# Performance work log

Measured on AMD Instinct MI355X. Metric: run time of the kernel, lower is better.

Reference implementation:

```python
import jax, jax.numpy as jnp
import numpy as np

BS, LX, LY, H, MD = 16, 1024, 1024, 512, 512


def setup_inputs() -> dict:
    key = jax.random.key(0)
    ks = jax.random.split(key, 8)
    x = jax.random.normal(ks[0], (BS, LX, H), dtype=jnp.float32)
    y = jax.random.normal(ks[1], (BS, LY, H), dtype=jnp.float32)
    y_mask = jax.random.bernoulli(ks[2], 0.2, (BS, LY))  # True = masked
    s1 = 1.0 / np.sqrt(H)
    W1 = jax.random.uniform(ks[3], (MD, H), jnp.float32, -s1, s1)
    b1 = jax.random.uniform(ks[4], (MD,), jnp.float32, -s1, s1)
    W2 = jax.random.uniform(ks[5], (MD, H), jnp.float32, -s1, s1)
    b2 = jax.random.uniform(ks[6], (MD,), jnp.float32, -s1, s1)
    s2 = 1.0 / np.sqrt(MD)
    k7, k8 = jax.random.split(ks[7])
    w_o = jax.random.uniform(k7, (MD,), jnp.float32, -s2, s2)
    b_o = jax.random.uniform(k8, (), jnp.float32, -s2, s2)
    return {"x": x, "y": y, "y_mask": y_mask, "W1": W1, "b1": b1,
            "W2": W2, "b2": b2, "w_o": w_o, "b_o": b_o}


def reference(x, y, y_mask, W1, b1, W2, b2, w_o, b_o):
    # Projections: [B,L,MD]
    x_proj = jax.nn.relu(jnp.einsum('blh,mh->blm', x, W1) + b1)
    y_proj = jax.nn.relu(jnp.einsum('blh,mh->blm', y, W2) + b2)
    # o_liner is linear, so o_liner(x_i + y_j) = w_o.x_i + w_o.y_j + b_o
    sx = x_proj @ w_o  # [B,Lx]
    sy = y_proj @ w_o  # [B,Ly]
    scores = sx[:, :, None] + sy[:, None, :] + b_o  # [B,Lx,Ly]
    scores = jnp.where(y_mask[:, None, :], jnp.float32(-1e7), scores)
    alpha = jax.nn.softmax(scores, axis=-1)  # softmax over len_y
    return alpha
```

## Files before the change

kernel.cpp:

```cpp
#include <hip/hip_runtime.h>
#include <hip/hip_bf16.h>

#define BS 16
#define LX 1024
#define LY 1024
#define H 512
#define MD 512
#define RY (BS * LY)

typedef __attribute__((ext_vector_type(8))) __bf16 bf16x8;
typedef __attribute__((ext_vector_type(4))) float floatx4;

__device__ __forceinline__ void load_lds16(const __bf16* g, __bf16* l) {
    __builtin_amdgcn_global_load_lds(
        (const __attribute__((address_space(1))) void*)g,
        (__attribute__((address_space(3))) void*)l,
        16, 0, 0);
}

__global__ __launch_bounds__(256) void prep_w2(const float* __restrict__ W2,
                                               __bf16* __restrict__ wb) {
    const int i = blockIdx.x * 256 + threadIdx.x;
    const float4 a = *(const float4*)(W2 + (size_t)i * 8);
    const float4 b = *(const float4*)(W2 + (size_t)i * 8 + 4);
    bf16x8 v = { (__bf16)a.x, (__bf16)a.y, (__bf16)a.z, (__bf16)a.w,
                 (__bf16)b.x, (__bf16)b.y, (__bf16)b.z, (__bf16)b.w };
    *(bf16x8*)(wb + (size_t)i * 8) = v;
}

#define BM 64
#define BN 128
#define BKT 64
__global__ __launch_bounds__(256) void gemm_sy(const float* __restrict__ Y,
                                               const __bf16* __restrict__ wb,
                                               const float* __restrict__ b2,
                                               const float* __restrict__ wo,
                                               float* __restrict__ part) {
    __shared__ __align__(16) __bf16 Bs[BN * BKT];

    const int tid  = threadIdx.x;
    const int lane = tid & 63;
    const int wave = tid >> 6;
    const int wm = wave >> 1;
    const int wn = wave & 1;
    const int la = lane & 15;
    const int qa = lane >> 4;

    const int id = blockIdx.x;
    const int mt = ((id >> 5) << 3) | (id & 7);
    const int nt = (id >> 3) & 3;
    const int m0 = mt * BM, n0 = nt * BN;

    const int lrow = lane >> 3;
    const int lcol = (lane & 7) * 8;

    const float* yrow0 = Y + (size_t)(m0 + wm * 32 + la) * H + qa * 8;
    const float* yrow1 = yrow0 + 16 * H;

    floatx4 acc[2][4] = {};

    for (int k0 = 0; k0 < H; k0 += BKT) {
        float4 a00 = *(const float4*)(yrow0 + k0);
        float4 a01 = *(const float4*)(yrow0 + k0 + 4);
        float4 a02 = *(const float4*)(yrow0 + k0 + 32);
        float4 a03 = *(const float4*)(yrow0 + k0 + 36);
        float4 a10 = *(const float4*)(yrow1 + k0);
        float4 a11 = *(const float4*)(yrow1 + k0 + 4);
        float4 a12 = *(const float4*)(yrow1 + k0 + 32);
        float4 a13 = *(const float4*)(yrow1 + k0 + 36);

        __syncthreads();
        #pragma unroll
        for (int r = 0; r < 4; ++r) {
            const int rb = r * 32 + wave * 8;
            load_lds16(wb + (size_t)(n0 + rb + lrow) * H + k0 + lcol, &Bs[rb * BKT]);
        }

        bf16x8 afr[2][2];
        afr[0][0] = { (__bf16)a00.x, (__bf16)a00.y, (__bf16)a00.z, (__bf16)a00.w,
                      (__bf16)a01.x, (__bf16)a01.y, (__bf16)a01.z, (__bf16)a01.w };
        afr[0][1] = { (__bf16)a02.x, (__bf16)a02.y, (__bf16)a02.z, (__bf16)a02.w,
                      (__bf16)a03.x, (__bf16)a03.y, (__bf16)a03.z, (__bf16)a03.w };
        afr[1][0] = { (__bf16)a10.x, (__bf16)a10.y, (__bf16)a10.z, (__bf16)a10.w,
                      (__bf16)a11.x, (__bf16)a11.y, (__bf16)a11.z, (__bf16)a11.w };
        afr[1][1] = { (__bf16)a12.x, (__bf16)a12.y, (__bf16)a12.z, (__bf16)a12.w,
                      (__bf16)a13.x, (__bf16)a13.y, (__bf16)a13.z, (__bf16)a13.w };

        __syncthreads();

        #pragma unroll
        for (int kh = 0; kh < 2; ++kh) {
            bf16x8 bfr[4];
            #pragma unroll
            for (int nf = 0; nf < 4; ++nf)
                bfr[nf] = *(const bf16x8*)&Bs[(wn * 64 + nf * 16 + la) * BKT + kh * 32 + qa * 8];
            #pragma unroll
            for (int mf = 0; mf < 2; ++mf)
                #pragma unroll
                for (int nf = 0; nf < 4; ++nf)
                    acc[mf][nf] = __builtin_amdgcn_mfma_f32_16x16x32_bf16(afr[mf][kh], bfr[nf], acc[mf][nf], 0, 0, 0);
        }
    }

    const int slice = nt * 2 + wn;
    #pragma unroll
    for (int mf = 0; mf < 2; ++mf) {
        #pragma unroll
        for (int reg = 0; reg < 4; ++reg) {
            float s = 0.f;
            #pragma unroll
            for (int nf = 0; nf < 4; ++nf) {
                const int n = n0 + wn * 64 + nf * 16 + la;
                float v = acc[mf][nf][reg] + b2[n];
                v = fmaxf(v, 0.f);
                s += v * wo[n];
            }
            s += __shfl_xor(s, 1);
            s += __shfl_xor(s, 2);
            s += __shfl_xor(s, 4);
            s += __shfl_xor(s, 8);
            if (la == 0) {
                const int m = m0 + wm * 32 + mf * 16 + qa * 4 + reg;
                part[(size_t)slice * RY + m] = s;
            }
        }
    }
}

__global__ __launch_bounds__(256) void softmax_p(const float* __restrict__ part,
                                                 const int* __restrict__ mask,
                                                 float* __restrict__ p) {
    const int b = blockIdx.x;
    const int tid = threadIdx.x;
    __shared__ float red[8];

    float vals[4];
    int   ms[4];
    float mx = -INFINITY;
    #pragma unroll
    for (int c = 0; c < 4; ++c) {
        const int j = c * 256 + tid;
        float v = 0.f;
        #pragma unroll
        for (int t = 0; t < 8; ++t) v += part[t * RY + b * LY + j];
        vals[c] = v;
        ms[c]   = mask[b * LY + j];
        if (!ms[c]) mx = fmaxf(mx, v);
    }
    #pragma unroll
    for (int off = 1; off < 64; off <<= 1) mx = fmaxf(mx, __shfl_xor(mx, off));
    if ((tid & 63) == 0) red[tid >> 6] = mx;
    __syncthreads();
    mx = fmaxf(fmaxf(red[0], red[1]), fmaxf(red[2], red[3]));

    float e[4];
    float sum = 0.f;
    #pragma unroll
    for (int c = 0; c < 4; ++c) {
        e[c] = ms[c] ? 0.f : __expf(vals[c] - mx);
        sum += e[c];
    }
    #pragma unroll
    for (int off = 1; off < 64; off <<= 1) sum += __shfl_xor(sum, off);
    if ((tid & 63) == 0) red[4 + (tid >> 6)] = sum;
    __syncthreads();
    sum = red[4] + red[5] + red[6] + red[7];
    const float inv = 1.0f / sum;

    #pragma unroll
    for (int c = 0; c < 4; ++c)
        p[b * LY + c * 256 + tid] = e[c] * inv;
}

__global__ __launch_bounds__(256) void bcast(const float* __restrict__ p,
                                             float4* __restrict__ out) {
    const int tid = threadIdx.x;
    const long base_row = (long)blockIdx.x * 8;
    const int b = (int)(base_row >> 10);
    const float4 v = *(const float4*)(p + b * LY + tid * 4);
    float4* o = out + base_row * (LY / 4) + tid;
    #pragma unroll
    for (int r = 0; r < 8; ++r) o[r * (LY / 4)] = v;
}

extern "C" void kernel_launch(void* const* d_in, const int* in_sizes, int n_in,
                              void* d_out, int out_size, void* d_ws, size_t ws_size,
                              hipStream_t stream) {
    const float* y  = (const float*)d_in[1];
    const int*   ym = (const int*)  d_in[2];
    const float* W2 = (const float*)d_in[5];
    const float* b2 = (const float*)d_in[6];
    const float* wo = (const float*)d_in[7];

    char* ws = (char*)d_ws;
    __bf16* wb   = (__bf16*)ws;
    float*  part = (float*)(ws + (size_t)MD * H * 2);
    float*  p    = part + 8 * RY;

    prep_w2<<<(MD * H) / (256 * 8), 256, 0, stream>>>(W2, wb);
    gemm_sy<<<(MD / BN) * (RY / BM), 256, 0, stream>>>(y, wb, b2, wo, part);
    softmax_p<<<BS, 256, 0, stream>>>(part, ym, p);
    bcast<<<(BS * LX) / 8, 256, 0, stream>>>(p, (float4*)d_out);
}
```

Measured before the change: 162.2 us.

## Double-buffer W2 tiles in LDS and XOR-swizzle layout to avoid bank conflicts

```diff
diff --git a/kernel.cpp b/kernel.cpp
--- a/kernel.cpp
+++ b/kernel.cpp
@@ -31,12 +31,13 @@
 #define BM 64
 #define BN 128
 #define BKT 64
+#define NK (H / BKT)
 __global__ __launch_bounds__(256) void gemm_sy(const float* __restrict__ Y,
                                                const __bf16* __restrict__ wb,
                                                const float* __restrict__ b2,
                                                const float* __restrict__ wo,
                                                float* __restrict__ part) {
-    __shared__ __align__(16) __bf16 Bs[BN * BKT];
+    __shared__ __align__(16) __bf16 Bs[2][BN * BKT];
 
     const int tid  = threadIdx.x;
     const int lane = tid & 63;
@@ -52,48 +53,61 @@
     const int m0 = mt * BM, n0 = nt * BN;
 
     const int lrow = lane >> 3;
-    const int lcol = (lane & 7) * 8;
+    const int lcol = (((lane & 7) ^ lrow) * 8);
 
     const float* yrow0 = Y + (size_t)(m0 + wm * 32 + la) * H + qa * 8;
     const float* yrow1 = yrow0 + 16 * H;
 
     floatx4 acc[2][4] = {};
-
-    for (int k0 = 0; k0 < H; k0 += BKT) {
-        float4 a00 = *(const float4*)(yrow0 + k0);
-        float4 a01 = *(const float4*)(yrow0 + k0 + 4);
-        float4 a02 = *(const float4*)(yrow0 + k0 + 32);
-        float4 a03 = *(const float4*)(yrow0 + k0 + 36);
-        float4 a10 = *(const float4*)(yrow1 + k0);
-        float4 a11 = *(const float4*)(yrow1 + k0 + 4);
-        float4 a12 = *(const float4*)(yrow1 + k0 + 32);
-        float4 a13 = *(const float4*)(yrow1 + k0 + 36);
-
+    float4 a[8];
+
+    a[0] = *(const float4*)(yrow0);      a[1] = *(const float4*)(yrow0 + 4);
+    a[2] = *(const float4*)(yrow0 + 32); a[3] = *(const float4*)(yrow0 + 36);
+    a[4] = *(const float4*)(yrow1);      a[5] = *(const float4*)(yrow1 + 4);
+    a[6] = *(const float4*)(yrow1 + 32); a[7] = *(const float4*)(yrow1 + 36);
+    #pragma unroll
+    for (int r = 0; r < 4; ++r) {
+        const int rb = r * 32 + wave * 8;
+        load_lds16(wb + (size_t)(n0 + rb + lrow) * H + lcol, &Bs[0][rb * BKT]);
+    }
+
+    for (int k = 0; k < NK; ++k) {
+        const int cur = k & 1;
         __syncthreads();
-        #pragma unroll
-        for (int r = 0; r < 4; ++r) {
-            const int rb = r * 32 + wave * 8;
-            load_lds16(wb + (size_t)(n0 + rb + lrow) * H + k0 + lcol, &Bs[rb * BKT]);
+
+        bf16x8 afr[2][2];
+        afr[0][0] = { (__bf16)a[0].x, (__bf16)a[0].y, (__bf16)a[0].z, (__bf16)a[0].w,
+                      (__bf16)a[1].x, (__bf16)a[1].y, (__bf16)a[1].z, (__bf16)a[1].w };
+        afr[0][1] = { (__bf16)a[2].x, (__bf16)a[2].y, (__bf16)a[2].z, (__bf16)a[2].w,
+                      (__bf16)a[3].x, (__bf16)a[3].y, (__bf16)a[3].z, (__bf16)a[3].w };
+        afr[1][0] = { (__bf16)a[4].x, (__bf16)a[4].y, (__bf16)a[4].z, (__bf16)a[4].w,
+                      (__bf16)a[5].x, (__bf16)a[5].y, (__bf16)a[5].z, (__bf16)a[5].w };
+        afr[1][1] = { (__bf16)a[6].x, (__bf16)a[6].y, (__bf16)a[6].z, (__bf16)a[6].w,
+                      (__bf16)a[7].x, (__bf16)a[7].y, (__bf16)a[7].z, (__bf16)a[7].w };
+
+        if (k + 1 < NK) {
+            const int k1 = (k + 1) * BKT;
+            #pragma unroll
+            for (int r = 0; r < 4; ++r) {
+                const int rb = r * 32 + wave * 8;
+                load_lds16(wb + (size_t)(n0 + rb + lrow) * H + k1 + lcol,
+                           &Bs[1 - cur][rb * BKT]);
+            }
+            a[0] = *(const float4*)(yrow0 + k1);      a[1] = *(const float4*)(yrow0 + k1 + 4);
+            a[2] = *(const float4*)(yrow0 + k1 + 32); a[3] = *(const float4*)(yrow0 + k1 + 36);
+            a[4] = *(const float4*)(yrow1 + k1);      a[5] = *(const float4*)(yrow1 + k1 + 4);
+            a[6] = *(const float4*)(yrow1 + k1 + 32); a[7] = *(const float4*)(yrow1 + k1 + 36);
         }
-
-        bf16x8 afr[2][2];
-        afr[0][0] = { (__bf16)a00.x, (__bf16)a00.y, (__bf16)a00.z, (__bf16)a00.w,
-                      (__bf16)a01.x, (__bf16)a01.y, (__bf16)a01.z, (__bf16)a01.w };
-        afr[0][1] = { (__bf16)a02.x, (__bf16)a02.y, (__bf16)a02.z, (__bf16)a02.w,
-                      (__bf16)a03.x, (__bf16)a03.y, (__bf16)a03.z, (__bf16)a03.w };
-        afr[1][0] = { (__bf16)a10.x, (__bf16)a10.y, (__bf16)a10.z, (__bf16)a10.w,
-                      (__bf16)a11.x, (__bf16)a11.y, (__bf16)a11.z, (__bf16)a11.w };
-        afr[1][1] = { (__bf16)a12.x, (__bf16)a12.y, (__bf16)a12.z, (__bf16)a12.w,
-                      (__bf16)a13.x, (__bf16)a13.y, (__bf16)a13.z, (__bf16)a13.w };
-
-        __syncthreads();
 
         #pragma unroll
         for (int kh = 0; kh < 2; ++kh) {
             bf16x8 bfr[4];
             #pragma unroll
-            for (int nf = 0; nf < 4; ++nf)
-                bfr[nf] = *(const bf16x8*)&Bs[(wn * 64 + nf * 16 + la) * BKT + kh * 32 + qa * 8];
+            for (int nf = 0; nf < 4; ++nf) {
+                const int row  = wn * 64 + nf * 16 + la;
+                const int slot = (kh * 4 + qa) ^ (la & 7);
+                bfr[nf] = *(const bf16x8*)&Bs[cur][row * BKT + slot * 8];
+            }
             #pragma unroll
             for (int mf = 0; mf < 2; ++mf)
                 #pragma unroll
```

Result: no change. 165.1 us (+1.8%).
